# Kernel optimization log

Measured on AMD Instinct MI355X. Metric: run time of the kernel, lower is better.

The kernel has to match this reference:

```python
import jax, jax.numpy as jnp
import numpy as np
import math

B, S, D, H, L, F = 32, 512, 512, 8, 4, 2048
DK = D // H
EPS = 1e-5


def _cosine_pos_emb(seq_len, d_model):
    pe = np.zeros((seq_len, d_model), dtype=np.float32)
    position = np.arange(seq_len, dtype=np.float32)[:, None]
    div_term = np.exp(np.arange(0, d_model, 2, dtype=np.float32) * (-math.log(10000.0) / d_model))
    pe[:, 0::2] = np.sin(position * div_term)
    pe[:, 1::2] = np.cos(position * div_term)
    return jnp.asarray(pe[None])  # (1, S, D)


def setup_inputs() -> dict:
    key = jax.random.key(0)
    ks = jax.random.split(key, 12)
    w = 0.02
    return {
        "q_embed_data": jax.random.normal(ks[0], (B, S, D), jnp.float32),
        "qa_embed_data": jax.random.normal(ks[1], (B, S, D), jnp.float32),
        "forget_rate": jax.random.uniform(ks[2], (B, S, 1), jnp.float32),
        "pos_emb": _cosine_pos_emb(S, D),
        # per-layer stacked params (torch Linear convention: W is (out,in))
        "Wk": w * jax.random.normal(ks[3], (L, D, D), jnp.float32),
        "bk": jnp.zeros((L, D), jnp.float32),
        "Wv": w * jax.random.normal(ks[4], (L, D, D), jnp.float32),
        "bv": jnp.zeros((L, D), jnp.float32),
        "Wo": w * jax.random.normal(ks[5], (L, D, D), jnp.float32),
        "bo": jnp.zeros((L, D), jnp.float32),
        "W1": w * jax.random.normal(ks[6], (L, F, D), jnp.float32),
        "b1": jnp.zeros((L, F), jnp.float32),
        "W2": w * jax.random.normal(ks[7], (L, D, F), jnp.float32),
        "b2": jnp.zeros((L, D), jnp.float32),
        "ln1_g": jnp.ones((L, D), jnp.float32),
        "ln1_b": jnp.zeros((L, D), jnp.float32),
        "ln2_g": jnp.ones((L, D), jnp.float32),
        "ln2_b": jnp.zeros((L, D), jnp.float32),
    }


def _layer_norm(x, g, b):
    mu = jnp.mean(x, axis=-1, keepdims=True)
    var = jnp.mean(jnp.square(x - mu), axis=-1, keepdims=True)
    return (x - mu) * jax.lax.rsqrt(var + EPS) * g + b


def _forward(q_embed_data, qa_embed_data, forget_rate, pos_emb,
             Wk, bk, Wv, bv, Wo, bo, W1, b1, W2, b2,
             ln1_g, ln1_b, ln2_g, ln2_b):
    x = q_embed_data + pos_emb   # queries/keys stream
    y = qa_embed_data + pos_emb  # values stream (fixed across layers)
    scale = 1.0 / math.sqrt(DK)
    # mask=0 path: triu(k=0)==0 -> strictly past positions only (j < i)
    allowed = jnp.tril(jnp.ones((S, S), dtype=bool), k=-1)
    fr = forget_rate[:, None, :, :]  # (B,1,S,1): row-wise decay on scores
    neg = jnp.asarray(-1e32, x.dtype)

    def block(x, p):
        wk, bk_, wv, bv_, wo, bo_, w1, b1_, w2, b2_, g1, be1, g2, be2 = p
        # kq_same=1: q and k share the k_linear projection (so q == k here)
        kq = (jnp.einsum('bsd,ed->bse', x, wk) + bk_).reshape(B, S, H, DK).transpose(0, 2, 1, 3)
        v = (jnp.einsum('bsd,ed->bse', y, wv) + bv_).reshape(B, S, H, DK).transpose(0, 2, 1, 3)
        scores = jnp.einsum('bhsd,bhtd->bhst', kq, kq) * scale
        scores = scores * fr
        scores = jnp.where(allowed, scores, neg)
        attn = jax.nn.softmax(scores, axis=-1)
        attn = attn.at[:, :, 0, :].set(0.0)  # zero_pad: first query row zeroed
        ctx = jnp.einsum('bhst,bhtd->bhsd', attn, v).transpose(0, 2, 1, 3).reshape(B, S, D)
        out = jnp.einsum('bsd,ed->bse', ctx, wo) + bo_
        x = _layer_norm(x + out, g1, be1)
        ff = jnp.einsum('bsf,df->bsd', jax.nn.relu(jnp.einsum('bsd,fd->bsf', x, w1) + b1_), w2) + b2_
        x = _layer_norm(x + ff, g2, be2)
        return x, None

    x, _ = jax.lax.scan(block, x, (Wk, bk, Wv, bv, Wo, bo, W1, b1, W2, b2, ln1_g, ln1_b, ln2_g, ln2_b))
    return x


def reference(q_embed_data, qa_embed_data, forget_rate, pos_emb,
              Wk, bk, Wv, bv, Wo, bo, W1, b1, W2, b2,
              ln1_g, ln1_b, ln2_g, ln2_b):
    return _forward(q_embed_data, qa_embed_data, forget_rate, pos_emb,
                    Wk, bk, Wv, bv, Wo, bo, W1, b1, W2, b2,
                    ln1_g, ln1_b, ln2_g, ln2_b)
```

## Files before the change

kernel.cpp:

```cpp
#include <hip/hip_runtime.h>
#include <hip/hip_bf16.h>

constexpr int B_ = 32, S_ = 512, D_ = 512, H_ = 8, L_ = 4, F_ = 2048, DK_ = 64;

typedef __attribute__((ext_vector_type(8))) short short8;
typedef __attribute__((ext_vector_type(4))) float f32x4;

__device__ inline unsigned short f2b(float f) {
  union { __hip_bfloat16 h; unsigned short u; } cv;
  cv.h = __float2bfloat16(f);
  return cv.u;
}
__device__ inline float b2f(unsigned short u) {
  union { unsigned int i; float f; } c;
  c.i = ((unsigned int)u) << 16;
  return c.f;
}
__device__ inline float waveReduceSum(float v) {
  #pragma unroll
  for (int o = 32; o > 0; o >>= 1) v += __shfl_xor(v, o);
  return v;
}

__global__ void prep_kernel(const float4* __restrict__ q, const float4* __restrict__ qa,
                            const float4* __restrict__ pos, float4* __restrict__ xf,
                            uint2* __restrict__ xb, uint2* __restrict__ yb) {
  int i = blockIdx.x * blockDim.x + threadIdx.x;
  float4 p = pos[i & 65535];
  float4 a = q[i], c = qa[i];
  float4 xv, yv;
  xv.x = a.x + p.x; xv.y = a.y + p.y; xv.z = a.z + p.z; xv.w = a.w + p.w;
  yv.x = c.x + p.x; yv.y = c.y + p.y; yv.z = c.z + p.z; yv.w = c.w + p.w;
  xf[i] = xv;
  uint2 px, py;
  px.x = (unsigned)f2b(xv.x) | ((unsigned)f2b(xv.y) << 16);
  px.y = (unsigned)f2b(xv.z) | ((unsigned)f2b(xv.w) << 16);
  py.x = (unsigned)f2b(yv.x) | ((unsigned)f2b(yv.y) << 16);
  py.y = (unsigned)f2b(yv.z) | ((unsigned)f2b(yv.w) << 16);
  xb[i] = px;
  yb[i] = py;
}

__global__ void cast_kernel(const float4* __restrict__ src, uint2* __restrict__ dst, int n4) {
  int i = blockIdx.x * blockDim.x + threadIdx.x;
  if (i >= n4) return;
  float4 v = src[i];
  uint2 p;
  p.x = (unsigned)f2b(v.x) | ((unsigned)f2b(v.y) << 16);
  p.y = (unsigned)f2b(v.z) | ((unsigned)f2b(v.w) << 16);
  dst[i] = p;
}

template<int BM, int RELU, int STORE>
__global__ __launch_bounds__(512, 2) void gemm256_kernel(
    const __hip_bfloat16* __restrict__ A,
    const __hip_bfloat16* __restrict__ W,
    const float* __restrict__ bias,
    const __hip_bfloat16* __restrict__ A2,
    const __hip_bfloat16* __restrict__ W2,
    const float* __restrict__ bias2,
    __hip_bfloat16* __restrict__ Cb,
    __hip_bfloat16* __restrict__ Cb2,
    int Ndim, int Kdim, int kLen)
{
  constexpr int ABUF = BM * 128;
  constexpr int BBASE = 2 * ABUF;
  constexpr int M_REP = BM / 32;
  __shared__ char lds[BBASE + 65536];
  const int tid = threadIdx.x, wave = tid >> 6, lane = tid & 63;
  const int rl = lane & 15, gq = lane >> 4;
  const int wr = wave >> 2, wc = wave & 3;

  const int nwg = gridDim.x * gridDim.y;
  const int lin = blockIdx.y * gridDim.x + blockIdx.x;
  const int swz = (lin & 7) * (nwg >> 3) + (lin >> 3);
  const int bx = swz % gridDim.x, by = swz / gridDim.x;

  const int row0 = by * BM;
  const int col0 = bx * 256;

  const __hip_bfloat16* Ap = A;
  const __hip_bfloat16* Wp = W;
  const float* bp = bias;
  int kOff = blockIdx.z * kLen;
  if (STORE == 3) {
    kOff = 0;
    if (blockIdx.z) { Ap = A2; Wp = W2; bp = bias2; }
  }

  f32x4 acc[M_REP][4] = {};
  const int ntiles = kLen >> 6;

  auto stage = [&](int kt, int d) {
    const int kbase = kOff + (kt << 6);
    #pragma unroll
    for (int r = 0; r < BM / 64; ++r) {
      int p = r * 8192 + wave * 1024 + lane * 16;
      int R = p >> 7, q = (p >> 4) & 7;
      int gc = q ^ (R & 7);
      const __hip_bfloat16* src = Ap + (size_t)(row0 + R) * Kdim + kbase + gc * 8;
      __builtin_amdgcn_global_load_lds(
          (const __attribute__((address_space(1))) void*)src,
          (__attribute__((address_space(3))) void*)(lds + d * ABUF + p), 16, 0, 0);
    }
    #pragma unroll
    for (int r = 0; r < 4; ++r) {
      int p = r * 8192 + wave * 1024 + lane * 16;
      int R = p >> 7, q = (p >> 4) & 7;
      int gc = q ^ (R & 7);
      const __hip_bfloat16* src = Wp + (size_t)(col0 + R) * Kdim + kbase + gc * 8;
      __builtin_amdgcn_global_load_lds(
          (const __attribute__((address_space(1))) void*)src,
          (__attribute__((address_space(3))) void*)(lds + BBASE + d * 32768 + p), 16, 0, 0);
    }
  };

  stage(0, 0);
  for (int kt = 0; kt < ntiles; ++kt) {
    const int d = kt & 1;
    asm volatile("s_waitcnt vmcnt(0)" ::: "memory");
    __builtin_amdgcn_sched_barrier(0);
    __syncthreads();
    if (kt + 1 < ntiles) stage(kt + 1, d ^ 1);
    __builtin_amdgcn_sched_barrier(0);

    #pragma unroll
    for (int ph = 0; ph < 4; ++ph) {
      constexpr int MH = M_REP / 2;
      const int mh = ph >> 1, nh = ph & 1;
      short8 aF[MH][2], bF[2][2];
      #pragma unroll
      for (int mi = 0; mi < MH; ++mi) {
        int r = wr * (BM / 2) + (mh * MH + mi) * 16 + rl;
        #pragma unroll
        for (int kf = 0; kf < 2; ++kf)
          aF[mi][kf] = *(const short8*)(lds + d * ABUF + r * 128 +
                                        (((kf * 4 + gq) ^ (r & 7)) << 4));
      }
      #pragma unroll
      for (int ni = 0; ni < 2; ++ni) {
        int r = wc * 64 + (nh * 2 + ni) * 16 + rl;
        #pragma unroll
        for (int kf = 0; kf < 2; ++kf)
          bF[ni][kf] = *(const short8*)(lds + BBASE + d * 32768 + r * 128 +
                                        (((kf * 4 + gq) ^ (r & 7)) << 4));
      }
      __builtin_amdgcn_s_setprio(1);
      #pragma unroll
      for (int mi = 0; mi < MH; ++mi)
        #pragma unroll
        for (int ni = 0; ni < 2; ++ni)
          #pragma unroll
          for (int kf = 0; kf < 2; ++kf)
            acc[mh * MH + mi][nh * 2 + ni] = __builtin_amdgcn_mfma_f32_16x16x32_bf16(
                aF[mi][kf], bF[ni][kf], acc[mh * MH + mi][nh * 2 + ni], 0, 0, 0);
      __builtin_amdgcn_s_setprio(0);
    }
  }

  __syncthreads();
  char* sw = lds + wave * (BM * 64);
  const bool vt = (STORE == 2) || (STORE == 3 && blockIdx.z == 1);
  const bool addb = (STORE == 3) ? true : ((bias != nullptr) && (blockIdx.z == 0));
  float bvv[4];
  #pragma unroll
  for (int n = 0; n < 4; ++n)
    bvv[n] = addb ? bp[col0 + wc * 64 + n * 16 + rl] : 0.0f;

  #pragma unroll
  for (int n = 0; n < 4; ++n)
    #pragma unroll
    for (int m = 0; m < M_REP; ++m)
      #pragma unroll
      for (int j = 0; j < 4; ++j) {
        float val = acc[m][n][j] + bvv[n];
        if (RELU) val = fmaxf(val, 0.0f);
        int addr;
        if (vt) {
          int orow = n * 16 + rl, ocol = m * 16 + gq * 4 + j;
          addr = orow * 128 + ((ocol * 2) ^ ((orow & 7) << 4));
        } else {
          int orow = m * 16 + gq * 4 + j;
          addr = orow * 128 + (((n * 16 + rl) * 2) ^ (((orow >> 1) & 7) << 4));
        }
        *(unsigned short*)(sw + addr) = f2b(val);
      }
  asm volatile("s_waitcnt lgkmcnt(0)" ::: "memory");
  __builtin_amdgcn_sched_barrier(0);

  __hip_bfloat16* Cbd = blockIdx.z ? Cb2 : Cb;
  const int cchunk = lane & 7;
  if (vt) {
    const int bh64 = ((row0 >> 9) * 8 + (col0 >> 6) + wc) * 64;
    const int tbase = (row0 & 511) + wr * 64;
    #pragma unroll
    for (int it = 0; it < 8; ++it) {
      int d0 = it * 8 + (lane >> 3);
      uint4 vv = *(const uint4*)(sw + d0 * 128 + ((cchunk * 16) ^ ((d0 & 7) << 4)));
      *(uint4*)((char*)Cbd + ((size_t)(bh64 + d0) * 512 + tbase) * 2 + cchunk * 16) = vv;
    }
  } else {
    #pragma unroll
    for (int it = 0; it < BM / 16; ++it) {
      int orow = it * 8 + (lane >> 3);
      uint4 vv = *(const uint4*)(sw + orow * 128 + ((cchunk * 16) ^ (((orow >> 1) & 7) << 4)));
      *(uint4*)((char*)Cbd + ((size_t)(row0 + wr * (BM / 2) + orow) * Ndim + col0 + wc * 64) * 2 +
                cchunk * 16) = vv;
    }
  }
}

__global__ __launch_bounds__(256, 2) void fattn_kernel(
    const __hip_bfloat16* __restrict__ kq,
    const __hip_bfloat16* __restrict__ vT,
    const float* __restrict__ fr,
    __hip_bfloat16* __restrict__ ctx)
{
  __shared__ char lds[40960];
  const int tid = threadIdx.x, wave = tid >> 6, lane = tid & 63;
  const int rl = lane & 15, gq = lane >> 4;
  const int lin = blockIdx.x;
  const int qb = (3 - (lin >> 8)) * 128;
  const int wpi = lin & 255;
  const int bh = (wpi & 7) * 32 + (wpi >> 3);
  const int b = bh >> 3, h = bh & 7;
  const size_t kqbase = ((size_t)b * S_) * D_ + h * DK_;
  const size_t vtbase = ((size_t)bh * DK_) * S_;
  const int qw0 = qb + wave * 32;
  const int qw_end = qw0 + 32;

  short8 qA[2][2];
  #pragma unroll
  for (int qf = 0; qf < 2; ++qf)
    #pragma unroll
    for (int kf = 0; kf < 2; ++kf)
      qA[qf][kf] = *(const short8*)(kq + kqbase + (size_t)(qw0 + qf * 16 + rl) * D_ + kf * 32 + gq * 8);

  float sfv[2][4];
  #pragma unroll
  for (int qf = 0; qf < 2; ++qf)
    #pragma unroll
    for (int j = 0; j < 4; ++j)
      sfv[qf][j] = fr[b * S_ + qw0 + qf * 16 + gq * 4 + j] * 0.125f;

  f32x4 o[2][4] = {};
  float mrow[2][4], lrow[2][4];
  #pragma unroll
  for (int qf = 0; qf < 2; ++qf)
    #pragma unroll
    for (int j = 0; j < 4; ++j) { mrow[qf][j] = -3.0e38f; lrow[qf][j] = 0.0f; }

  int sgoff[2], sldsoff[2];
  #pragma unroll
  for (int c = 0; c < 2; ++c) {
    int p = (wave * 2 + c) * 1024 + lane * 16;
    int r = p >> 7;
    int ch = (p >> 4) & 7;
    sgoff[c] = r * 1024 + ((ch ^ (r & 7)) << 4);
    sldsoff[c] = (wave * 2 + c) * 1024;
  }
  const char* kgbase = (const char*)kq + kqbase * 2;
  const char* vgbase = (const char*)vT + vtbase * 2;

  auto stage = [&](int ti, int d) {
    const int t0 = ti << 6;
    #pragma unroll
    for (int c = 0; c < 2; ++c) {
      __builtin_amdgcn_global_load_lds(
          (const __attribute__((address_space(1))) void*)(kgbase + (size_t)t0 * 1024 + sgoff[c]),
          (__attribute__((address_space(3))) void*)(lds + d * 8192 + sldsoff[c]), 16, 0, 0);
      __builtin_amdgcn_global_load_lds(
          (const __attribute__((address_space(1))) void*)(vgbase + t0 * 2 + sgoff[c]),
          (__attribute__((address_space(3))) void*)(lds + 16384 + d * 8192 + sldsoff[c]), 16, 0, 0);
    }
  };

  const int nt = (qb + 128) >> 6;
  stage(0, 0);
  for (int ti = 0; ti < nt; ++ti) {
    const int t0 = ti << 6;
    const int d = ti & 1;
    if (ti + 1 < nt) {
      stage(ti + 1, d ^ 1);
      asm volatile("s_waitcnt vmcnt(4)" ::: "memory");
    } else {
      asm volatile("s_waitcnt vmcnt(0)" ::: "memory");
    }
    __builtin_amdgcn_sched_barrier(0);
    __syncthreads();

    if (t0 < qw_end) {
      short8 kB[4][2];
      #pragma unroll
      for (int tf = 0; tf < 4; ++tf)
        #pragma unroll
        for (int kf = 0; kf < 2; ++kf) {
          int r = tf * 16 + rl;
          kB[tf][kf] = *(const short8*)(lds + d * 8192 + r * 128 + (((kf * 4 + gq) ^ (r & 7)) << 4));
        }
      short8 vB[4][2];
      #pragma unroll
      for (int df = 0; df < 4; ++df)
        #pragma unroll
        for (int kf = 0; kf < 2; ++kf) {
          int r = df * 16 + rl;
          vB[df][kf] = *(const short8*)(lds + 16384 + d * 8192 + r * 128 + (((kf * 4 + gq) ^ (r & 7)) << 4));
        }

      #pragma unroll
      for (int qf = 0; qf < 2; ++qf) {
        f32x4 c4[4] = {};
        #pragma unroll
        for (int tf = 0; tf < 4; ++tf)
          #pragma unroll
          for (int kf = 0; kf < 2; ++kf)
            c4[tf] = __builtin_amdgcn_mfma_f32_16x16x32_bf16(qA[qf][kf], kB[tf][kf], c4[tf], 0, 0, 0);

        const int qg0 = qw0 + qf * 16 + gq * 4;
        #pragma unroll
        for (int tf = 0; tf < 4; ++tf) {
          int tg = t0 + tf * 16 + rl;
          #pragma unroll
          for (int j = 0; j < 4; ++j) {
            float s = c4[tf][j] * sfv[qf][j];
            c4[tf][j] = (tg >= qg0 + j) ? -3.0e38f : s;
          }
        }
        float tm[4];
        #pragma unroll
        for (int j = 0; j < 4; ++j) {
          tm[j] = fmaxf(fmaxf(c4[0][j], c4[1][j]), fmaxf(c4[2][j], c4[3][j]));
          #pragma unroll
          for (int msk = 1; msk < 16; msk <<= 1) tm[j] = fmaxf(tm[j], __shfl_xor(tm[j], msk));
        }
        #pragma unroll
        for (int j = 0; j < 4; ++j) {
          float mn = fmaxf(mrow[qf][j], tm[j]);
          float fac = __expf(mrow[qf][j] - mn);
          mrow[qf][j] = mn;
          lrow[qf][j] *= fac;
          #pragma unroll
          for (int df = 0; df < 4; ++df) o[qf][df][j] *= fac;
        }
        float rs[4] = {0.f, 0.f, 0.f, 0.f};
        #pragma unroll
        for (int tf = 0; tf < 4; ++tf) {
          int tloc = tf * 16 + rl;
          #pragma unroll
          for (int j = 0; j < 4; ++j) {
            float e = __expf(c4[tf][j] - mrow[qf][j]);
            rs[j] += e;
            int qloc = gq * 4 + j;
            int addr = 32768 + wave * 2048 + qloc * 128 +
                       ((((tloc >> 3) ^ (qloc & 7)) << 4)) + (tloc & 7) * 2;
            *(unsigned short*)(lds + addr) = f2b(e);
          }
        }
        #pragma unroll
        for (int j = 0; j < 4; ++j) {
          float r = rs[j];
          #pragma unroll
          for (int msk = 1; msk < 16; msk <<= 1) r += __shfl_xor(r, msk);
          lrow[qf][j] += r;
        }
        asm volatile("s_waitcnt lgkmcnt(0)" ::: "memory");
        __builtin_amdgcn_sched_barrier(0);
        short8 pA[2];
        #pragma unroll
        for (int kf = 0; kf < 2; ++kf)
          pA[kf] = *(const short8*)(lds + 32768 + wave * 2048 + rl * 128 +
                                    (((kf * 4 + gq) ^ (rl & 7)) << 4));
        #pragma unroll
        for (int df = 0; df < 4; ++df)
          #pragma unroll
          for (int kf = 0; kf < 2; ++kf)
            o[qf][df] = __builtin_amdgcn_mfma_f32_16x16x32_bf16(pA[kf], vB[df][kf], o[qf][df], 0, 0, 0);
      }
    }
    __syncthreads();
  }

  #pragma unroll
  for (int qf = 0; qf < 2; ++qf)
    #pragma unroll
    for (int j = 0; j < 4; ++j) {
      int qg = qw0 + qf * 16 + gq * 4 + j;
      float inv = (qg == 0) ? 0.0f : 1.0f / lrow[qf][j];
      #pragma unroll
      for (int df = 0; df < 4; ++df) {
        union { __hip_bfloat16 hh; unsigned short u; } cv;
        cv.u = f2b(o[qf][df][j] * inv);
        ctx[((size_t)(b * S_ + qg)) * D_ + h * DK_ + df * 16 + rl] = cv.hh;
      }
    }
}

template<int NADD>
__global__ __launch_bounds__(256) void ln_kernel(
    const float4* __restrict__ xin, const uint4* __restrict__ add,
    const uint4* __restrict__ add2,
    const float* __restrict__ g, const float* __restrict__ bta,
    float4* xf_out, uint2* __restrict__ xb_out)
{
  const int lane = threadIdx.x & 63, wv = threadIdx.x >> 6;
  const size_t row = (size_t)blockIdx.x * 4 + wv;
  const size_t base4 = row * 128;

  float4 x0 = xin[base4 + lane * 2], x1 = xin[base4 + lane * 2 + 1];
  uint4 ab = add[row * 64 + lane];
  const unsigned short* ap = (const unsigned short*)&ab;
  float v[8];
  v[0] = x0.x; v[1] = x0.y; v[2] = x0.z; v[3] = x0.w;
  v[4] = x1.x; v[5] = x1.y; v[6] = x1.z; v[7] = x1.w;
  #pragma unroll
  for (int i = 0; i < 8; ++i) v[i] += b2f(ap[i]);
  if (NADD == 2) {
    uint4 ab2 = add2[row * 64 + lane];
    const unsigned short* ap2 = (const unsigned short*)&ab2;
    #pragma unroll
    for (int i = 0; i < 8; ++i) v[i] += b2f(ap2[i]);
  }
  float s = 0.0f;
  #pragma unroll
  for (int i = 0; i < 8; ++i) s += v[i];
  s = waveReduceSum(s);
  float mu = s * (1.0f / 512.0f);
  float vs = 0.0f;
  #pragma unroll
  for (int i = 0; i < 8; ++i) { float dd = v[i] - mu; vs += dd * dd; }
  vs = waveReduceSum(vs);
  float rstd = rsqrtf(vs * (1.0f / 512.0f) + 1e-5f);

  const int c0i = lane * 8;
  float4 gg0 = *(const float4*)(g + c0i), gg1 = *(const float4*)(g + c0i + 4);
  float4 bb0 = *(const float4*)(bta + c0i), bb1 = *(const float4*)(bta + c0i + 4);
  float o[8];
  o[0] = (v[0] - mu) * rstd * gg0.x + bb0.x;
  o[1] = (v[1] - mu) * rstd * gg0.y + bb0.y;
  o[2] = (v[2] - mu) * rstd * gg0.z + bb0.z;
  o[3] = (v[3] - mu) * rstd * gg0.w + bb0.w;
  o[4] = (v[4] - mu) * rstd * gg1.x + bb1.x;
  o[5] = (v[5] - mu) * rstd * gg1.y + bb1.y;
  o[6] = (v[6] - mu) * rstd * gg1.z + bb1.z;
  o[7] = (v[7] - mu) * rstd * gg1.w + bb1.w;
  float4 w0, w1;
  w0.x = o[0]; w0.y = o[1]; w0.z = o[2]; w0.w = o[3];
  w1.x = o[4]; w1.y = o[5]; w1.z = o[6]; w1.w = o[7];
  xf_out[base4 + lane * 2] = w0;
  xf_out[base4 + lane * 2 + 1] = w1;
  uint2 p0, p1;
  p0.x = (unsigned)f2b(o[0]) | ((unsigned)f2b(o[1]) << 16);
  p0.y = (unsigned)f2b(o[2]) | ((unsigned)f2b(o[3]) << 16);
  p1.x = (unsigned)f2b(o[4]) | ((unsigned)f2b(o[5]) << 16);
  p1.y = (unsigned)f2b(o[6]) | ((unsigned)f2b(o[7]) << 16);
  xb_out[row * 128 + lane * 2] = p0;
  xb_out[row * 128 + lane * 2 + 1] = p1;
}

extern "C" void kernel_launch(void* const* d_in, const int* in_sizes, int n_in,
                              void* d_out, int out_size, void* d_ws, size_t ws_size,
                              hipStream_t stream) {
  (void)in_sizes; (void)n_in; (void)out_size; (void)ws_size;
  const float* q   = (const float*)d_in[0];
  const float* qa  = (const float*)d_in[1];
  const float* frr = (const float*)d_in[2];
  const float* pos = (const float*)d_in[3];
  const float* Wk  = (const float*)d_in[4];
  const float* bk  = (const float*)d_in[5];
  const float* Wv  = (const float*)d_in[6];
  const float* bv  = (const float*)d_in[7];
  const float* Wo  = (const float*)d_in[8];
  const float* bo  = (const float*)d_in[9];
  const float* W1  = (const float*)d_in[10];
  const float* b1  = (const float*)d_in[11];
  const float* W2  = (const float*)d_in[12];
  const float* b2  = (const float*)d_in[13];
  const float* g1  = (const float*)d_in[14];
  const float* be1 = (const float*)d_in[15];
  const float* g2  = (const float*)d_in[16];
  const float* be2 = (const float*)d_in[17];

  char* ws = (char*)d_ws;
  float*          xf   = (float*)(ws + 0);
  __hip_bfloat16* xb   = (__hip_bfloat16*)(ws + 33554432);
  __hip_bfloat16* yb   = (__hip_bfloat16*)(ws + 50331648);
  __hip_bfloat16* kqb  = (__hip_bfloat16*)(ws + 67108864);
  __hip_bfloat16* vtb  = (__hip_bfloat16*)(ws + 83886080);
  __hip_bfloat16* ctxb = (__hip_bfloat16*)(ws + 100663296);
  __hip_bfloat16* hb   = (__hip_bfloat16*)(ws + 117440512);
  __hip_bfloat16* wkb  = (__hip_bfloat16*)(ws + 184549376);
  __hip_bfloat16* wvb  = (__hip_bfloat16*)(ws + 186646528);
  __hip_bfloat16* wob  = (__hip_bfloat16*)(ws + 188743680);
  __hip_bfloat16* w1b  = (__hip_bfloat16*)(ws + 190840832);
  __hip_bfloat16* w2b  = (__hip_bfloat16*)(ws + 199229440);
  __hip_bfloat16* obf = (__hip_bfloat16*)(ws + 67108864);
  __hip_bfloat16* pf0 = (__hip_bfloat16*)(ws + 83886080);
  __hip_bfloat16* pf1 = (__hip_bfloat16*)(ws + 100663296);

  prep_kernel<<<8192, 256, 0, stream>>>((const float4*)q, (const float4*)qa,
                                        (const float4*)pos, (float4*)xf,
                                        (uint2*)xb, (uint2*)yb);
  cast_kernel<<<1024, 256, 0, stream>>>((const float4*)Wk, (uint2*)wkb, 262144);
  cast_kernel<<<1024, 256, 0, stream>>>((const float4*)Wv, (uint2*)wvb, 262144);
  cast_kernel<<<1024, 256, 0, stream>>>((const float4*)Wo, (uint2*)wob, 262144);
  cast_kernel<<<4096, 256, 0, stream>>>((const float4*)W1, (uint2*)w1b, 1048576);
  cast_kernel<<<4096, 256, 0, stream>>>((const float4*)W2, (uint2*)w2b, 1048576);

  for (int l = 0; l < L_; ++l) {
    gemm256_kernel<128,0,3><<<dim3(2, 128, 2), 512, 0, stream>>>(
        xb, wkb + (size_t)l * 262144, bk + l * 512,
        yb, wvb + (size_t)l * 262144, bv + l * 512,
        kqb, vtb, 512, 512, 512);
    fattn_kernel<<<1024, 256, 0, stream>>>(kqb, vtb, frr, ctxb);
    gemm256_kernel<128,0,0><<<dim3(2, 128, 1), 512, 0, stream>>>(
        ctxb, wob + (size_t)l * 262144, bo + l * 512,
        nullptr, nullptr, nullptr, obf, nullptr, 512, 512, 512);
    ln_kernel<1><<<4096, 256, 0, stream>>>((const float4*)xf, (const uint4*)obf, nullptr,
                                           g1 + l * 512, be1 + l * 512,
                                           (float4*)xf, (uint2*)xb);
    gemm256_kernel<256,1,0><<<dim3(8, 64, 1), 512, 0, stream>>>(
        xb, w1b + (size_t)l * 1048576, b1 + l * 2048,
        nullptr, nullptr, nullptr, hb, nullptr, 2048, 512, 512);
    gemm256_kernel<256,0,0><<<dim3(2, 64, 2), 512, 0, stream>>>(
        hb, w2b + (size_t)l * 1048576, b2 + l * 512,
        nullptr, nullptr, nullptr, pf0, pf1, 512, 2048, 1024);
    float* lnout = (l == L_ - 1) ? (float*)d_out : xf;
    ln_kernel<2><<<4096, 256, 0, stream>>>((const float4*)xf, (const uint4*)pf0,
                                           (const uint4*)pf1,
                                           g2 + l * 512, be2 + l * 512,
                                           (float4*)lnout, (uint2*)xb);
  }
}
```

Baseline: 824.3 us.

## Use 4-stage BK=32 LDS pipeline in GEMM and raw barriers

Result: no change. 836.9 us (+1.5%).

```diff
diff --git a/kernel.cpp b/kernel.cpp
--- a/kernel.cpp
+++ b/kernel.cpp
@@ -63,10 +63,11 @@
     __hip_bfloat16* __restrict__ Cb2,
     int Ndim, int Kdim, int kLen)
 {
-  constexpr int ABUF = BM * 128;
-  constexpr int BBASE = 2 * ABUF;
+  constexpr int ABUF = BM * 64;
+  constexpr int WREG = 4 * ABUF;
   constexpr int M_REP = BM / 32;
-  __shared__ char lds[BBASE + 65536];
+  constexpr int LPT = BM / 128 + 2;
+  __shared__ char lds[WREG + 65536];
   const int tid = threadIdx.x, wave = tid >> 6, lane = tid & 63;
   const int rl = lane & 15, gq = lane >> 4;
   const int wr = wave >> 2, wc = wave & 3;
@@ -89,73 +90,68 @@
   }
 
   f32x4 acc[M_REP][4] = {};
-  const int ntiles = kLen >> 6;
-
-  auto stage = [&](int kt, int d) {
-    const int kbase = kOff + (kt << 6);
-    #pragma unroll
-    for (int r = 0; r < BM / 64; ++r) {
-      int p = r * 8192 + wave * 1024 + lane * 16;
-      int R = p >> 7, q = (p >> 4) & 7;
-      int gc = q ^ (R & 7);
+  const int ntiles = kLen >> 5;
+
+  auto stage = [&](int kt) {
+    const int buf = kt & 3;
+    const int kbase = kOff + (kt << 5);
+    #pragma unroll
+    for (int r = 0; r < BM / 128; ++r) {
+      int p = r * 8192 + tid * 16;
+      int R = p >> 6, c = (p >> 4) & 3;
+      int gc = c ^ ((R >> 1) & 3);
       const __hip_bfloat16* src = Ap + (size_t)(row0 + R) * Kdim + kbase + gc * 8;
       __builtin_amdgcn_global_load_lds(
           (const __attribute__((address_space(1))) void*)src,
-          (__attribute__((address_space(3))) void*)(lds + d * ABUF + p), 16, 0, 0);
-    }
-    #pragma unroll
-    for (int r = 0; r < 4; ++r) {
-      int p = r * 8192 + wave * 1024 + lane * 16;
-      int R = p >> 7, q = (p >> 4) & 7;
-      int gc = q ^ (R & 7);
+          (__attribute__((address_space(3))) void*)(lds + buf * ABUF + p), 16, 0, 0);
+    }
+    #pragma unroll
+    for (int r = 0; r < 2; ++r) {
+      int p = r * 8192 + tid * 16;
+      int R = p >> 6, c = (p >> 4) & 3;
+      int gc = c ^ ((R >> 1) & 3);
       const __hip_bfloat16* src = Wp + (size_t)(col0 + R) * Kdim + kbase + gc * 8;
       __builtin_amdgcn_global_load_lds(
           (const __attribute__((address_space(1))) void*)src,
-          (__attribute__((address_space(3))) void*)(lds + BBASE + d * 32768 + p), 16, 0, 0);
+          (__attribute__((address_space(3))) void*)(lds + WREG + buf * 16384 + p), 16, 0, 0);
     }
   };
 
-  stage(0, 0);
+  stage(0); stage(1); stage(2);
   for (int kt = 0; kt < ntiles; ++kt) {
-    const int d = kt & 1;
-    asm volatile("s_waitcnt vmcnt(0)" ::: "memory");
+    if (kt + 2 < ntiles) {
+      asm volatile("s_waitcnt vmcnt(%0)" :: "n"(2 * LPT) : "memory");
+    } else if (kt + 1 < ntiles) {
+      asm volatile("s_waitcnt vmcnt(%0)" :: "n"(LPT) : "memory");
+    } else {
+      asm volatile("s_waitcnt vmcnt(0)" ::: "memory");
+    }
     __builtin_amdgcn_sched_barrier(0);
-    __syncthreads();
-    if (kt + 1 < ntiles) stage(kt + 1, d ^ 1);
+    __builtin_amdgcn_s_barrier();
     __builtin_amdgcn_sched_barrier(0);
-
-    #pragma unroll
-    for (int ph = 0; ph < 4; ++ph) {
-      constexpr int MH = M_REP / 2;
-      const int mh = ph >> 1, nh = ph & 1;
-      short8 aF[MH][2], bF[2][2];
+    if (kt + 3 < ntiles) stage(kt + 3);
+
+    const int abase = (kt & 3) * ABUF;
+    const int wbase = WREG + (kt & 3) * 16384;
+    short8 bF[4];
+    #pragma unroll
+    for (int n = 0; n < 4; ++n) {
+      int rr = wc * 64 + n * 16 + rl;
+      bF[n] = *(const short8*)(lds + wbase + rr * 64 + ((gq ^ ((rr >> 1) & 3)) << 4));
+    }
+    short8 aF[M_REP];
+    #pragma unroll
+    for (int m = 0; m < M_REP; ++m) {
+      int rr = wr * (BM / 2) + m * 16 + rl;
+      aF[m] = *(const short8*)(lds + abase + rr * 64 + ((gq ^ ((rr >> 1) & 3)) << 4));
+    }
+    __builtin_amdgcn_s_setprio(1);
+    #pragma unroll
+    for (int m = 0; m < M_REP; ++m)
       #pragma unroll
-      for (int mi = 0; mi < MH; ++mi) {
-        int r = wr * (BM / 2) + (mh * MH + mi) * 16 + rl;
-        #pragma unroll
-        for (int kf = 0; kf < 2; ++kf)
-          aF[mi][kf] = *(const short8*)(lds + d * ABUF + r * 128 +
-                                        (((kf * 4 + gq) ^ (r & 7)) << 4));
-      }
-      #pragma unroll
-      for (int ni = 0; ni < 2; ++ni) {
-        int r = wc * 64 + (nh * 2 + ni) * 16 + rl;
-        #pragma unroll
-        for (int kf = 0; kf < 2; ++kf)
-          bF[ni][kf] = *(const short8*)(lds + BBASE + d * 32768 + r * 128 +
-                                        (((kf * 4 + gq) ^ (r & 7)) << 4));
-      }
-      __builtin_amdgcn_s_setprio(1);
-      #pragma unroll
-      for (int mi = 0; mi < MH; ++mi)
-        #pragma unroll
-        for (int ni = 0; ni < 2; ++ni)
-          #pragma unroll
-          for (int kf = 0; kf < 2; ++kf)
-            acc[mh * MH + mi][nh * 2 + ni] = __builtin_amdgcn_mfma_f32_16x16x32_bf16(
-                aF[mi][kf], bF[ni][kf], acc[mh * MH + mi][nh * 2 + ni], 0, 0, 0);
-      __builtin_amdgcn_s_setprio(0);
-    }
+      for (int n = 0; n < 4; ++n)
+        acc[m][n] = __builtin_amdgcn_mfma_f32_16x16x32_bf16(aF[m], bF[n], acc[m][n], 0, 0, 0);
+    __builtin_amdgcn_s_setprio(0);
   }
 
   __syncthreads();
@@ -287,7 +283,8 @@
       asm volatile("s_waitcnt vmcnt(0)" ::: "memory");
     }
     __builtin_amdgcn_sched_barrier(0);
-    __syncthreads();
+    __builtin_amdgcn_s_barrier();
+    __builtin_amdgcn_sched_barrier(0);
 
     if (t0 < qw_end) {
       short8 kB[4][2];
@@ -377,7 +374,9 @@
             o[qf][df] = __builtin_amdgcn_mfma_f32_16x16x32_bf16(pA[kf], vB[df][kf], o[qf][df], 0, 0, 0);
       }
     }
-    __syncthreads();
+    __builtin_amdgcn_sched_barrier(0);
+    __builtin_amdgcn_s_barrier();
+    __builtin_amdgcn_sched_barrier(0);
   }
 
   #pragma unroll
```
